# Kernel tuning notes

Hardware: AMD Instinct MI355X
Metric: run time of the kernel (lower is better)

Reference implementation:

```python
import jax, jax.numpy as jnp
import numpy as np

TIME_DIM = 2
DIM = 512
N_ENT = 100000
N_REL = 500
B = 512
K = 128
MARGIN = 2.0
EPS = 1e-6


def proj_tan0(u):
    # tangent space at origin o=(1,0,...,0): first coordinate zeroed
    return u.at[..., 0].set(0.0)


def expmap0(u):
    # exponential map at the origin of the pseudo-hyperboloid Q^{s,t}, beta=-1.
    # quadratic norm of tangent vector (time dims negative): branch on sign.
    u = proj_tan0(u)
    a = -jnp.sum(u[..., :TIME_DIM] ** 2, axis=-1) + jnp.sum(u[..., TIME_DIM:] ** 2, axis=-1)
    sp = jnp.sqrt(jnp.clip(a, EPS))   # space-like branch radius
    st = jnp.sqrt(jnp.clip(-a, EPS))  # time-like branch radius
    c = jnp.where(a > 0, jnp.cosh(sp), jnp.cos(st))
    s = jnp.where(a > 0, jnp.sinh(sp) / sp, jnp.sin(st) / st)
    o = jnp.zeros_like(u).at[..., 0].set(1.0)
    return c[..., None] * o + s[..., None] * u


def _norm_givens(r):
    g = r.reshape(r.shape[0], -1, 2)
    return g / jnp.clip(jnp.linalg.norm(g, axis=-1, keepdims=True), 1e-15)


def givens_rotations(r, x):
    g = _norm_givens(r)
    xp = x.reshape(r.shape[0], -1, 2)
    c, s = g[..., 0:1], g[..., 1:2]
    x0, x1 = xp[..., 0:1], xp[..., 1:2]
    out = jnp.concatenate([c * x0 - s * x1, c * x1 + s * x0], axis=-1)
    return out.reshape(r.shape[0], -1)


def givens_reflection(r, x):
    g = _norm_givens(r)
    xp = x.reshape(r.shape[0], -1, 2)
    c, s = g[..., 0:1], g[..., 1:2]
    x0, x1 = xp[..., 0:1], xp[..., 1:2]
    out = jnp.concatenate([c * x0 + s * x1, s * x0 - c * x1], axis=-1)
    return out.reshape(r.shape[0], -1)


def manhattan_sqdist(x, y):
    # Manhattan-style geodesic on Q^{s,t} via the S^{t-1} x H^s decomposition:
    # leg 1: rotate time direction on the sphere of radius ||x_t||,
    # leg 2: hyperbolic distance along the shared time direction. Asymmetric
    # in (x, y), hence the min over both orders in the caller.
    xt, xs = x[..., :TIME_DIM], x[..., TIME_DIM:]
    yt, ys = y[..., :TIME_DIM], y[..., TIME_DIM:]
    nx = jnp.linalg.norm(xt, axis=-1)
    ny = jnp.linalg.norm(yt, axis=-1)
    cosang = jnp.clip(jnp.sum(xt * yt, axis=-1) / (nx * ny), -1.0 + EPS, 1.0 - EPS)
    d_sph = nx * jnp.arccos(cosang)
    inner = nx * ny - jnp.sum(xs * ys, axis=-1)
    d_hyp = jnp.arccosh(jnp.clip(inner, 1.0 + EPS))
    return (d_sph + d_hyp) ** 2


def setup_inputs() -> dict:
    key = jax.random.key(0)
    ks = jax.random.split(key, 8)
    emb_entity = jax.random.normal(ks[0], (N_ENT, DIM), jnp.float32)
    relation_boost = 1e-5 * jax.nn.softplus(jax.random.normal(ks[1], (N_REL, TIME_DIM), jnp.float32))
    relation_rot_left = 2.0 * jax.random.uniform(ks[2], (N_REL, DIM), jnp.float32) - 1.0
    relation_rot_right = 2.0 * jax.random.uniform(ks[3], (N_REL, DIM), jnp.float32) - 1.0
    bias_head = jnp.zeros((N_ENT,), jnp.float32)
    bias_tail = jnp.zeros((N_ENT,), jnp.float32)
    u_idx = jax.random.randint(ks[4], (B,), 0, N_ENT)
    r_idx = jax.random.randint(ks[5], (B,), 0, N_REL)
    v_idx = jax.random.randint(ks[6], (B, K), 0, N_ENT)
    return {"emb_entity": emb_entity, "relation_boost": relation_boost,
            "relation_rot_left": relation_rot_left, "relation_rot_right": relation_rot_right,
            "bias_head": bias_head, "bias_tail": bias_tail,
            "u_idx": u_idx, "r_idx": r_idx, "v_idx": v_idx}


def reference(emb_entity, relation_boost, relation_rot_left, relation_rot_right,
              bias_head, bias_tail, u_idx, r_idx, v_idx):
    head = emb_entity[u_idx]                       # [B, D]
    tail = emb_entity[v_idx]                       # [B, K, D]
    b = jax.nn.softplus(relation_boost[r_idx])     # [B, 2]
    r_left = relation_rot_left[r_idx]
    r_right = relation_rot_right[r_idx]

    head = expmap0(head)
    tail = expmap0(proj_tan0(tail))

    head = givens_rotations(r_right, head)

    # dense (D x D) Lorentz boost per example, faithful to the original matmul
    C = jnp.sqrt(1.0 + b ** 2)
    t_idx = jnp.arange(TIME_DIM)
    bt_idx = DIM - TIME_DIM + jnp.arange(TIME_DIM)
    m_idx = jnp.arange(TIME_DIM, DIM - TIME_DIM)
    boost = jnp.zeros((b.shape[0], DIM, DIM), head.dtype)
    boost = boost.at[:, t_idx, t_idx].set(C)
    boost = boost.at[:, bt_idx, bt_idx].set(C)
    boost = boost.at[:, t_idx, bt_idx].set(-b)
    boost = boost.at[:, bt_idx, t_idx].set(-b)
    boost = boost.at[:, m_idx, m_idx].set(1.0)
    head = jnp.einsum('bij,bj->bi', boost, head)

    head = givens_reflection(r_left, head)

    # pairwise manifold distance, min over the two Manhattan-path orders
    c1 = manhattan_sqdist(head[:, None, :], tail)  # [B, K]
    c2 = manhattan_sqdist(tail, head[:, None, :])
    dist = jnp.minimum(c1, c2)

    return MARGIN - dist + bias_head[u_idx][:, None] + bias_tail[v_idx]
```

## Files before the change

kernel.cpp:

```cpp
#include <hip/hip_runtime.h>
#include <math.h>

#define DIM_ 512
#define K_ 128
#define EPS_ 1e-6f
#define MARGIN_ 2.0f
#define PI_ 3.14159265358979f

__device__ __forceinline__ float frcp(float x) { return __builtin_amdgcn_rcpf(x); }

__device__ __forceinline__ float fast_acos(float x) {
    float ax = fabsf(x);
    float p = -0.0187293f;
    p = p * ax + 0.0742610f;
    p = p * ax - 0.2121144f;
    p = p * ax + 1.5707288f;
    float r = sqrtf(fmaxf(1.f - ax, 0.f)) * p;
    return x < 0.f ? PI_ - r : r;
}

__device__ __forceinline__ void fast_coshsinh(float x, float& c, float& s) {
    float e  = __expf(x);
    float ei = frcp(e);
    c = 0.5f * (e + ei);
    s = 0.5f * (e - ei);
}

__device__ __forceinline__ void expmap_cs(float a, float& c, float& s) {
    if (a > 0.f) {
        float sp = sqrtf(fmaxf(a, EPS_));
        float ch, sh;
        fast_coshsinh(sp, ch, sh);
        c = ch; s = sh * frcp(sp);
    } else {
        float st = sqrtf(fmaxf(-a, EPS_));
        c = __cosf(st);
        s = __sinf(st) * frcp(st);
    }
}

__device__ __forceinline__ void givens_rot(float gc, float gs, float& x0, float& x1) {
    float rn = frcp(fmaxf(sqrtf(gc * gc + gs * gs), 1e-15f));
    float c = gc * rn, s = gs * rn;
    float y0 = c * x0 - s * x1;
    float y1 = c * x1 + s * x0;
    x0 = y0; x1 = y1;
}

__device__ __forceinline__ void givens_ref(float gc, float gs, float& x0, float& x1) {
    float rn = frcp(fmaxf(sqrtf(gc * gc + gs * gs), 1e-15f));
    float c = gc * rn, s = gs * rn;
    float y0 = c * x0 + s * x1;
    float y1 = s * x0 - c * x1;
    x0 = y0; x1 = y1;
}

__global__ __launch_bounds__(256) void ultrae_kernel(
    const float* __restrict__ emb,
    const float* __restrict__ rel_boost,
    const float* __restrict__ rot_left,
    const float* __restrict__ rot_right,
    const float* __restrict__ bias_head,
    const float* __restrict__ bias_tail,
    const int* __restrict__ u_idx,
    const int* __restrict__ r_idx,
    const int* __restrict__ v_idx,
    float* __restrict__ out)
{
    const int b = blockIdx.x;
    const int lane = threadIdx.x & 63;
    const int wave = threadIdx.x >> 6;
    const int u = u_idx[b];
    const int r = r_idx[b];

    const int kbase = (blockIdx.y * 4 + wave) * 4;
    const int4 vv = *(const int4*)(v_idx + b * K_ + kbase);
    const int vi[4] = {vv.x, vv.y, vv.z, vv.w};
    float4 t0[4], t1[4];
#pragma unroll
    for (int i = 0; i < 4; ++i) {
        const float* trow = emb + (size_t)vi[i] * DIM_ + lane * 8;
        t0[i] = *(const float4*)trow;
        t1[i] = *(const float4*)(trow + 4);
    }

    const float* hrow = emb + (size_t)u * DIM_ + lane * 8;
    float4 h0 = *(const float4*)hrow;
    float4 h1 = *(const float4*)(hrow + 4);
    if (lane == 0) h0.x = 0.f;
    float ps = h0.x*h0.x + h0.y*h0.y + h0.z*h0.z + h0.w*h0.w
             + h1.x*h1.x + h1.y*h1.y + h1.z*h1.z + h1.w*h1.w;
#pragma unroll
    for (int off = 32; off >= 1; off >>= 1) ps += __shfl_xor(ps, off, 64);
    float u1 = __shfl(h0.y, 0, 64);
    float a = ps - 2.f * u1 * u1;
    float ch, sh;
    expmap_cs(a, ch, sh);
    h0.x *= sh; h0.y *= sh; h0.z *= sh; h0.w *= sh;
    h1.x *= sh; h1.y *= sh; h1.z *= sh; h1.w *= sh;
    if (lane == 0) h0.x = ch;

    {
        const float* rr = rot_right + (size_t)r * DIM_ + lane * 8;
        float4 g0 = *(const float4*)rr;
        float4 g1 = *(const float4*)(rr + 4);
        givens_rot(g0.x, g0.y, h0.x, h0.y);
        givens_rot(g0.z, g0.w, h0.z, h0.w);
        givens_rot(g1.x, g1.y, h1.x, h1.y);
        givens_rot(g1.z, g1.w, h1.z, h1.w);
    }

    {
        float bb0 = __logf(1.f + __expf(rel_boost[2*r]));
        float bb1 = __logf(1.f + __expf(rel_boost[2*r+1]));
        float C0 = sqrtf(1.f + bb0*bb0);
        float C1 = sqrtf(1.f + bb1*bb1);
        float e0   = __shfl(h0.x, 0, 64);
        float e1   = __shfl(h0.y, 0, 64);
        float e510 = __shfl(h1.z, 63, 64);
        float e511 = __shfl(h1.w, 63, 64);
        if (lane == 0) {
            h0.x = C0*e0 - bb0*e510;
            h0.y = C1*e1 - bb1*e511;
        }
        if (lane == 63) {
            h1.z = C0*e510 - bb0*e0;
            h1.w = C1*e511 - bb1*e1;
        }
    }

    {
        const float* rl = rot_left + (size_t)r * DIM_ + lane * 8;
        float4 g0 = *(const float4*)rl;
        float4 g1 = *(const float4*)(rl + 4);
        givens_ref(g0.x, g0.y, h0.x, h0.y);
        givens_ref(g0.z, g0.w, h0.z, h0.w);
        givens_ref(g1.x, g1.y, h1.x, h1.y);
        givens_ref(g1.z, g1.w, h1.z, h1.w);
    }

    float hf0 = __shfl(h0.x, 0, 64);
    float hf1 = __shfl(h0.y, 0, 64);
    float nx = sqrtf(hf0*hf0 + hf1*hf1);
    if (lane == 0) { h0.x = 0.f; h0.y = 0.f; }
    const float bh = bias_head[u];
    const float rnx = frcp(nx);

#pragma unroll
    for (int i = 0; i < 4; ++i) {
        float4 s0 = t0[i], s1 = t1[i];
        float tt1 = __shfl(s0.y, 0, 64);
        if (lane == 0) { s0.x = 0.f; s0.y = 0.f; }
        float q = s0.x*s0.x + s0.y*s0.y + s0.z*s0.z + s0.w*s0.w
                + s1.x*s1.x + s1.y*s1.y + s1.z*s1.z + s1.w*s1.w;
        float d = h0.x*s0.x + h0.y*s0.y + h0.z*s0.z + h0.w*s0.w
                + h1.x*s1.x + h1.y*s1.y + h1.z*s1.z + h1.w*s1.w;
#pragma unroll
        for (int off = 32; off >= 1; off >>= 1) {
            q += __shfl_xor(q, off, 64);
            d += __shfl_xor(d, off, 64);
        }
        float at = q - tt1 * tt1;
        float ct, st;
        expmap_cs(at, ct, st);
        float yt1 = st * tt1;
        float ny = sqrtf(ct*ct + yt1*yt1);
        float cosang = (hf0*ct + hf1*yt1) * rnx * frcp(ny);
        cosang = fminf(fmaxf(cosang, -1.f + EPS_), 1.f - EPS_);
        float dsph = fminf(nx, ny) * fast_acos(cosang);
        float inner = fmaxf(nx*ny - st*d, 1.f + EPS_);
        float dhyp = __logf(inner + sqrtf(inner - 1.f) * sqrtf(inner + 1.f));
        float dsum = dsph + dhyp;
        if (lane == 0) {
            out[b * K_ + kbase + i] = MARGIN_ - dsum*dsum + bh + bias_tail[vi[i]];
        }
    }
}

extern "C" void kernel_launch(void* const* d_in, const int* in_sizes, int n_in,
                              void* d_out, int out_size, void* d_ws, size_t ws_size,
                              hipStream_t stream) {
    const float* emb       = (const float*)d_in[0];
    const float* rel_boost = (const float*)d_in[1];
    const float* rot_left  = (const float*)d_in[2];
    const float* rot_right = (const float*)d_in[3];
    const float* bias_h    = (const float*)d_in[4];
    const float* bias_t    = (const float*)d_in[5];
    const int* u_idx       = (const int*)d_in[6];
    const int* r_idx       = (const int*)d_in[7];
    const int* v_idx       = (const int*)d_in[8];
    float* out = (float*)d_out;

    int B = in_sizes[6];
    dim3 grid(B, 8), block(256);
    hipLaunchKernelGGL(ultrae_kernel, grid, block, 0, stream,
                       emb, rel_boost, rot_left, rot_right,
                       bias_h, bias_t, u_idx, r_idx, v_idx, out);
}
```

Measured before the change: 279.4 us.

## Process eight tails per wave and reduce through LDS transpose

Each wave now handles eight tail entities instead of four, which halves the grid and halves how often the head expmap/rotation/boost chain is recomputed per tail. The per-tail 64-lane butterfly reductions are replaced by writing partial sums to padded LDS, reading them back transposed, and finishing with three shuffles, so the post-reduction transcendental math runs once per lane group rather than redundantly across the whole wave. This costs more registers for eight prefetched tail rows, which may lower occupancy, and adds LDS traffic.

```diff
diff --git a/kernel.cpp b/kernel.cpp
--- a/kernel.cpp
+++ b/kernel.cpp
@@ -6,6 +6,7 @@
 #define EPS_ 1e-6f
 #define MARGIN_ 2.0f
 #define PI_ 3.14159265358979f
+#define QSTRIDE 68
 
 __device__ __forceinline__ float frcp(float x) { return __builtin_amdgcn_rcpf(x); }
 
@@ -67,22 +68,33 @@
     const int* __restrict__ v_idx,
     float* __restrict__ out)
 {
+    __shared__ float lds_q[4][8 * QSTRIDE + 4];
+    __shared__ float lds_d[4][8 * QSTRIDE + 4];
+
     const int b = blockIdx.x;
     const int lane = threadIdx.x & 63;
     const int wave = threadIdx.x >> 6;
     const int u = u_idx[b];
     const int r = r_idx[b];
 
-    const int kbase = (blockIdx.y * 4 + wave) * 4;
-    const int4 vv = *(const int4*)(v_idx + b * K_ + kbase);
-    const int vi[4] = {vv.x, vv.y, vv.z, vv.w};
-    float4 t0[4], t1[4];
-#pragma unroll
-    for (int i = 0; i < 4; ++i) {
-        const float* trow = emb + (size_t)vi[i] * DIM_ + lane * 8;
-        t0[i] = *(const float4*)trow;
-        t1[i] = *(const float4*)(trow + 4);
-    }
+    const int kbase = (blockIdx.y * 4 + wave) * 8;
+    const int* vp = v_idx + b * K_ + kbase;
+    const int4 vv0 = *(const int4*)(vp);
+    const int4 vv1 = *(const int4*)(vp + 4);
+    const int vi[8] = {vv0.x, vv0.y, vv0.z, vv0.w, vv1.x, vv1.y, vv1.z, vv1.w};
+    float4 t0[8], t1[8];
+#pragma unroll
+    for (int j = 0; j < 8; ++j) {
+        const float* trow = emb + (size_t)vi[j] * DIM_ + lane * 8;
+        t0[j] = *(const float4*)trow;
+        t1[j] = *(const float4*)(trow + 4);
+    }
+
+    const int m = lane & 7;
+    const int g = lane >> 3;
+    const int vm = vp[m];
+    const float tt1 = emb[(size_t)vm * DIM_ + 1];
+    const float bt = bias_tail[vm];
 
     const float* hrow = emb + (size_t)u * DIM_ + lane * 8;
     float4 h0 = *(const float4*)hrow;
@@ -147,33 +159,44 @@
     const float rnx = frcp(nx);
 
 #pragma unroll
-    for (int i = 0; i < 4; ++i) {
-        float4 s0 = t0[i], s1 = t1[i];
-        float tt1 = __shfl(s0.y, 0, 64);
+    for (int j = 0; j < 8; ++j) {
+        float4 s0 = t0[j], s1 = t1[j];
         if (lane == 0) { s0.x = 0.f; s0.y = 0.f; }
-        float q = s0.x*s0.x + s0.y*s0.y + s0.z*s0.z + s0.w*s0.w
-                + s1.x*s1.x + s1.y*s1.y + s1.z*s1.z + s1.w*s1.w;
-        float d = h0.x*s0.x + h0.y*s0.y + h0.z*s0.z + h0.w*s0.w
-                + h1.x*s1.x + h1.y*s1.y + h1.z*s1.z + h1.w*s1.w;
-#pragma unroll
-        for (int off = 32; off >= 1; off >>= 1) {
-            q += __shfl_xor(q, off, 64);
-            d += __shfl_xor(d, off, 64);
-        }
-        float at = q - tt1 * tt1;
-        float ct, st;
-        expmap_cs(at, ct, st);
-        float yt1 = st * tt1;
-        float ny = sqrtf(ct*ct + yt1*yt1);
-        float cosang = (hf0*ct + hf1*yt1) * rnx * frcp(ny);
-        cosang = fminf(fmaxf(cosang, -1.f + EPS_), 1.f - EPS_);
-        float dsph = fminf(nx, ny) * fast_acos(cosang);
-        float inner = fmaxf(nx*ny - st*d, 1.f + EPS_);
-        float dhyp = __logf(inner + sqrtf(inner - 1.f) * sqrtf(inner + 1.f));
-        float dsum = dsph + dhyp;
-        if (lane == 0) {
-            out[b * K_ + kbase + i] = MARGIN_ - dsum*dsum + bh + bias_tail[vi[i]];
-        }
+        float qp = s0.x*s0.x + s0.y*s0.y + s0.z*s0.z + s0.w*s0.w
+                 + s1.x*s1.x + s1.y*s1.y + s1.z*s1.z + s1.w*s1.w;
+        float dp = h0.x*s0.x + h0.y*s0.y + h0.z*s0.z + h0.w*s0.w
+                 + h1.x*s1.x + h1.y*s1.y + h1.z*s1.z + h1.w*s1.w;
+        lds_q[wave][j * QSTRIDE + lane] = qp;
+        lds_d[wave][j * QSTRIDE + lane] = dp;
+    }
+
+    __builtin_amdgcn_wave_barrier();
+
+    float q = 0.f, d = 0.f;
+    const float* qa = &lds_q[wave][m * QSTRIDE + g];
+    const float* da = &lds_d[wave][m * QSTRIDE + g];
+#pragma unroll
+    for (int k = 0; k < 8; ++k) {
+        q += qa[8 * k];
+        d += da[8 * k];
+    }
+    q += __shfl_xor(q, 8, 64);  d += __shfl_xor(d, 8, 64);
+    q += __shfl_xor(q, 16, 64); d += __shfl_xor(d, 16, 64);
+    q += __shfl_xor(q, 32, 64); d += __shfl_xor(d, 32, 64);
+
+    float at = q - tt1 * tt1;
+    float ct, st;
+    expmap_cs(at, ct, st);
+    float yt1 = st * tt1;
+    float ny = sqrtf(ct*ct + yt1*yt1);
+    float cosang = (hf0*ct + hf1*yt1) * rnx * frcp(ny);
+    cosang = fminf(fmaxf(cosang, -1.f + EPS_), 1.f - EPS_);
+    float dsph = fminf(nx, ny) * fast_acos(cosang);
+    float inner = fmaxf(nx*ny - st*d, 1.f + EPS_);
+    float dhyp = __logf(inner + sqrtf(inner - 1.f) * sqrtf(inner + 1.f));
+    float dsum = dsph + dhyp;
+    if (lane < 8) {
+        out[b * K_ + kbase + m] = MARGIN_ - dsum*dsum + bh + bt;
     }
 }
 
@@ -192,7 +215,7 @@
     float* out = (float*)d_out;
 
     int B = in_sizes[6];
-    dim3 grid(B, 8), block(256);
+    dim3 grid(B, 4), block(256);
     hipLaunchKernelGGL(ultrae_kernel, grid, block, 0, stream,
                        emb, rel_boost, rot_left, rot_right,
                        bias_h, bias_t, u_idx, r_idx, v_idx, out);
```

New measurement: 273.4 us. 2.2% less time.
